# Performance work log

Hardware: AMD Instinct MI355X
Metric: run time of the kernel (lower is better)

The kernel has to match this reference:

```python
import jax, jax.numpy as jnp
import numpy as np

C = 1024
H = 16
DH = C // H
DFF = 4 * C
D = 1024  # cond_dim
B = 2
L = 2048
MAX_SCALE_MUL = float(np.log(100.0))
EPS = 1e-6


def _ln(x):
    # LayerNorm without affine, eps=1e-6
    m = jnp.mean(x, axis=-1, keepdims=True)
    xc = x - m
    var = jnp.mean(xc * xc, axis=-1, keepdims=True)
    return xc * jax.lax.rsqrt(var + EPS)


def setup_inputs() -> dict:
    key = jax.random.key(0)
    ks = jax.random.split(key, 16)
    s = 0.02
    return {
        "x": jax.random.normal(ks[0], (B, L, C), jnp.float32),
        "cond_BD": jax.random.normal(ks[1], (B, D), jnp.float32),
        "attn_bias": jax.random.normal(ks[2], (1, 1, L, L), jnp.float32) * 0.1,
        "qkv_w": jax.random.normal(ks[3], (3 * C, C), jnp.float32) * s,
        "q_bias": jnp.zeros((C,), jnp.float32),
        "v_bias": jnp.zeros((C,), jnp.float32),
        "scale_mul": jnp.full((1, H, 1, 1), np.log(4.0), jnp.float32),
        "proj_w": jax.random.normal(ks[4], (C, C), jnp.float32) * s,
        "proj_b": jnp.zeros((C,), jnp.float32),
        "fc1_w": jax.random.normal(ks[5], (DFF, C), jnp.float32) * s,
        "fc1_b": jnp.zeros((DFF,), jnp.float32),
        "fc2_w": jax.random.normal(ks[6], (C, DFF), jnp.float32) * s,
        "fc2_b": jnp.zeros((C,), jnp.float32),
        "ada_w": jax.random.normal(ks[7], (6 * C, D), jnp.float32) * s,
        "ada_b": jnp.zeros((6 * C,), jnp.float32),
    }


def _attention(x, attn_bias, qkv_w, q_bias, v_bias, scale_mul, proj_w, proj_b):
    b, l, c = x.shape
    bias = jnp.concatenate([q_bias, jnp.zeros_like(q_bias), v_bias])
    qkv = x @ qkv_w.T + bias  # [B,L,3C]
    qkv = qkv.reshape(b, l, 3, H, DH).transpose(2, 0, 3, 1, 4)  # [3,B,H,L,DH]
    q, k, v = qkv[0], qkv[1], qkv[2]
    sm = jnp.exp(jnp.minimum(scale_mul, MAX_SCALE_MUL))  # [1,H,1,1]
    q = q * jax.lax.rsqrt(jnp.sum(q * q, -1, keepdims=True).clip(1e-24)) * sm
    k = k * jax.lax.rsqrt(jnp.sum(k * k, -1, keepdims=True).clip(1e-24))
    attn = jnp.einsum("bhqd,bhkd->bhqk", q, k) + attn_bias
    attn = jax.nn.softmax(attn, axis=-1)
    out = jnp.einsum("bhqk,bhkd->bhqd", attn, v)
    out = out.transpose(0, 2, 1, 3).reshape(b, l, c)
    return out @ proj_w.T + proj_b


def reference(x, cond_BD, attn_bias, qkv_w, q_bias, v_bias, scale_mul,
              proj_w, proj_b, fc1_w, fc1_b, fc2_w, fc2_b, ada_w, ada_b):
    # adaLN modulation: SiLU -> Linear -> 6 chunks of C
    ada = jax.nn.silu(cond_BD) @ ada_w.T + ada_b  # [B,6C]
    ada = ada.reshape(-1, 1, 6, C)
    g1, g2, s1, s2, sh1, sh2 = [ada[:, :, i, :] for i in range(6)]  # each [B,1,C]
    # attention branch
    h = _ln(x) * (s1 + 1.0) + sh1
    x = x + _attention(h, attn_bias, qkv_w, q_bias, v_bias, scale_mul, proj_w, proj_b) * g1
    # FFN branch (GELU tanh approx)
    h = _ln(x) * (s2 + 1.0) + sh2
    h = jax.nn.gelu(h @ fc1_w.T + fc1_b, approximate=True) @ fc2_w.T + fc2_b
    x = x + h * g2
    return x
```

## Files before the change

### kernel.cpp

```cpp
#include <hip/hip_runtime.h>
#include <stdint.h>

#define Ll 2048
#define Mrows 4096
#define LOG2E 1.44269504088896f

typedef unsigned short u16;
typedef __attribute__((ext_vector_type(8))) short short8;
typedef __attribute__((ext_vector_type(4))) float f32x4;

#if __has_builtin(__builtin_amdgcn_exp2f)
#define EXP2F(x) __builtin_amdgcn_exp2f(x)
#else
#define EXP2F(x) exp2f(x)
#endif

__device__ __forceinline__ float b2f(u16 b) {
  union { float f; unsigned u; } x; x.u = ((unsigned)b) << 16; return x.f;
}
__device__ __forceinline__ u16 f2b(float v) {
  union { float f; unsigned u; } x; x.f = v;
  unsigned r = x.u + 0x7fffu + ((x.u >> 16) & 1u);
  return (u16)(r >> 16);
}

#define GLOAD_LDS16(gp, sp)                                                        \
  __builtin_amdgcn_global_load_lds(                                                \
      (__attribute__((address_space(1))) void*)(void*)(gp),                        \
      (__attribute__((address_space(3))) void*)(sp), 16, 0, 0)

__global__ __launch_bounds__(256) void k_convert_all(
    const float* __restrict__ s0, u16* __restrict__ d0,
    const float* __restrict__ s1, u16* __restrict__ d1,
    const float* __restrict__ s2, u16* __restrict__ d2,
    const float* __restrict__ s3, u16* __restrict__ d3,
    const float* __restrict__ s4, float* __restrict__ d4) {
  int i = blockIdx.x * 256 + threadIdx.x;
  if (i >= 3145728) {
    i -= 3145728;
    float4 v = ((const float4*)s4)[i];
    v.x *= LOG2E; v.y *= LOG2E; v.z *= LOG2E; v.w *= LOG2E;
    ((float4*)d4)[i] = v;
    return;
  }
  const float* s; u16* d; int off;
  if (i < 786432)       { s = s0; d = d0; off = 0; }
  else if (i < 1048576) { s = s1; d = d1; off = 786432; }
  else if (i < 2097152) { s = s2; d = d2; off = 1048576; }
  else                  { s = s3; d = d3; off = 2097152; }
  i -= off;
  const float4 v = ((const float4*)s)[i];
  ushort4 o;
  o.x = f2b(v.x); o.y = f2b(v.y); o.z = f2b(v.z); o.w = f2b(v.w);
  ((ushort4*)d)[i] = o;
}

__global__ __launch_bounds__(256) void k_ada(const float* __restrict__ cond,
                                             const float* __restrict__ aw,
                                             const float* __restrict__ ab,
                                             float* __restrict__ out) {
  const int wv = threadIdx.x >> 6, lane = threadIdx.x & 63;
  const int j = blockIdx.x * 4 + wv;
  const int b = j / 6144, jj = j % 6144;
  const float* wr = aw + (size_t)jj * 1024;
  const float* cr = cond + b * 1024;
  float acc = 0.f;
  for (int d = lane; d < 1024; d += 64) {
    const float cv = cr[d];
    acc += (cv / (1.f + __expf(-cv))) * wr[d];
  }
  for (int off = 32; off; off >>= 1) acc += __shfl_xor(acc, off);
  if (lane == 0) out[b * 6144 + jj] = acc + ab[jj];
}

__global__ __launch_bounds__(256) void k_ln_mod(const float* __restrict__ x,
                                                const float* __restrict__ ada,
                                                u16* __restrict__ out,
                                                int s_off, int sh_off) {
  const int row = blockIdx.x;
  const int b = row >> 11;
  const int t = threadIdx.x;
  const float4 xv = ((const float4*)(x + (size_t)row * 1024))[t];
  float s = xv.x + xv.y + xv.z + xv.w;
  float s2 = xv.x * xv.x + xv.y * xv.y + xv.z * xv.z + xv.w * xv.w;
  for (int off = 32; off; off >>= 1) { s += __shfl_xor(s, off); s2 += __shfl_xor(s2, off); }
  __shared__ float red[8];
  const int wv = t >> 6, lane = t & 63;
  if (lane == 0) { red[wv] = s; red[4 + wv] = s2; }
  __syncthreads();
  s = red[0] + red[1] + red[2] + red[3];
  s2 = red[4] + red[5] + red[6] + red[7];
  const float mean = s * (1.f / 1024.f);
  const float var = s2 * (1.f / 1024.f) - mean * mean;
  const float rstd = rsqrtf(var + 1e-6f);
  const float4 sv = ((const float4*)(ada + b * 6144 + s_off))[t];
  const float4 shv = ((const float4*)(ada + b * 6144 + sh_off))[t];
  ushort4 ov;
  ov.x = f2b((xv.x - mean) * rstd * (1.f + sv.x) + shv.x);
  ov.y = f2b((xv.y - mean) * rstd * (1.f + sv.y) + shv.y);
  ov.z = f2b((xv.z - mean) * rstd * (1.f + sv.z) + shv.z);
  ov.w = f2b((xv.w - mean) * rstd * (1.f + sv.w) + shv.w);
  ((ushort4*)(out + (size_t)row * 1024))[t] = ov;
}

__global__ __launch_bounds__(256) void k_resid_ln(const float* __restrict__ x,
                                                  const float* __restrict__ p0,
                                                  const float* __restrict__ p1,
                                                  const float* __restrict__ ada,
                                                  float* __restrict__ x2,
                                                  u16* __restrict__ out) {
  const int row = blockIdx.x;
  const int b = row >> 11;
  const int t = threadIdx.x;
  const float4 xv = ((const float4*)(x + (size_t)row * 1024))[t];
  const float4 pa = ((const float4*)(p0 + (size_t)row * 1024))[t];
  const float4 pb = ((const float4*)(p1 + (size_t)row * 1024))[t];
  const float4 gv = ((const float4*)(ada + b * 6144 + 0))[t];
  float4 v;
  v.x = xv.x + (pa.x + pb.x) * gv.x; v.y = xv.y + (pa.y + pb.y) * gv.y;
  v.z = xv.z + (pa.z + pb.z) * gv.z; v.w = xv.w + (pa.w + pb.w) * gv.w;
  ((float4*)(x2 + (size_t)row * 1024))[t] = v;
  float s = v.x + v.y + v.z + v.w;
  float s2 = v.x * v.x + v.y * v.y + v.z * v.z + v.w * v.w;
  for (int off = 32; off; off >>= 1) { s += __shfl_xor(s, off); s2 += __shfl_xor(s2, off); }
  __shared__ float red[8];
  const int wv = t >> 6, lane = t & 63;
  if (lane == 0) { red[wv] = s; red[4 + wv] = s2; }
  __syncthreads();
  s = red[0] + red[1] + red[2] + red[3];
  s2 = red[4] + red[5] + red[6] + red[7];
  const float mean = s * (1.f / 1024.f);
  const float var = s2 * (1.f / 1024.f) - mean * mean;
  const float rstd = rsqrtf(var + 1e-6f);
  const float4 sv = ((const float4*)(ada + b * 6144 + 3072))[t];
  const float4 shv = ((const float4*)(ada + b * 6144 + 5120))[t];
  ushort4 ov;
  ov.x = f2b((v.x - mean) * rstd * (1.f + sv.x) + shv.x);
  ov.y = f2b((v.y - mean) * rstd * (1.f + sv.y) + shv.y);
  ov.z = f2b((v.z - mean) * rstd * (1.f + sv.z) + shv.z);
  ov.w = f2b((v.w - mean) * rstd * (1.f + sv.w) + shv.w);
  ((ushort4*)(out + (size_t)row * 1024))[t] = ov;
}

__global__ __launch_bounds__(256) void k_final(const float* __restrict__ x2,
                                               const float* __restrict__ f0,
                                               const float* __restrict__ f1,
                                               const float* __restrict__ ada,
                                               float* __restrict__ out) {
  const int i = blockIdx.x * 256 + threadIdx.x;
  const int elem = i * 4;
  const int b = elem >> 21;
  const int c = elem & 1023;
  const float4 xv = ((const float4*)x2)[i];
  const float4 fa = ((const float4*)f0)[i];
  const float4 fb = ((const float4*)f1)[i];
  const float4 gv = *(const float4*)(ada + b * 6144 + 1024 + c);
  float4 ov;
  ov.x = xv.x + (fa.x + fb.x) * gv.x; ov.y = xv.y + (fa.y + fb.y) * gv.y;
  ov.z = xv.z + (fa.z + fb.z) * gv.z; ov.w = xv.w + (fa.w + fb.w) * gv.w;
  ((float4*)out)[i] = ov;
}

template <int OUT_BF16, int GELU_ACT>
__global__ __launch_bounds__(256, 2)
void k_gemm_bt(const u16* __restrict__ A, const u16* __restrict__ W,
               const float* __restrict__ bias, void* __restrict__ Cout,
               float* __restrict__ Cout2, int M, int N, int Kc) {
  __shared__ u16 As[128 * 64];
  __shared__ u16 Bs[128 * 64];
  const int tid = threadIdx.x;
  const int wv = tid >> 6;
  const int lane = tid & 63;
  const int q = lane >> 4;
  const int r = lane & 15;
  const int wm = (wv & 1) * 64;
  const int wn = (wv >> 1) * 64;
  const int m0 = blockIdx.x * 128;
  const int n0 = blockIdx.y * 128;
  const int K = Kc * gridDim.z;
  const int kt0 = blockIdx.z * Kc;

  f32x4 acc[4][4];
#pragma unroll
  for (int i = 0; i < 4; ++i)
#pragma unroll
    for (int j = 0; j < 4; ++j) acc[i][j] = (f32x4)0.0f;

  const int srow = tid >> 3;
  const int scol = (tid & 7) * 8;
  const u16* Ag = A + (size_t)(m0 + srow) * K + scol;
  const u16* Wg = W + (size_t)(n0 + srow) * K + scol;
  u16* AsBase = &As[wv * 512];
  u16* BsBase = &Bs[wv * 512];

  for (int kt = kt0; kt < kt0 + Kc; kt += 64) {
    __syncthreads();
#pragma unroll
    for (int p = 0; p < 4; ++p) {
      GLOAD_LDS16(Ag + (size_t)(p * 32) * K + kt, AsBase + p * 2048);
      GLOAD_LDS16(Wg + (size_t)(p * 32) * K + kt, BsBase + p * 2048);
    }
    __syncthreads();
#pragma unroll
    for (int kc = 0; kc < 2; ++kc) {
      short8 af[4], bfr[4];
#pragma unroll
      for (int i = 0; i < 4; ++i) {
        af[i] = *(const short8*)(As + (wm + i * 16 + r) * 64 + kc * 32 + q * 8);
        bfr[i] = *(const short8*)(Bs + (wn + i * 16 + r) * 64 + kc * 32 + q * 8);
      }
#pragma unroll
      for (int mi = 0; mi < 4; ++mi)
#pragma unroll
        for (int ni = 0; ni < 4; ++ni)
          acc[mi][ni] = __builtin_amdgcn_mfma_f32_16x16x32_bf16(af[mi], bfr[ni],
                                                                acc[mi][ni], 0, 0, 0);
    }
  }
  float* Cf = (blockIdx.z == 0) ? (float*)Cout : Cout2;
#pragma unroll
  for (int mi = 0; mi < 4; ++mi) {
#pragma unroll
    for (int ni = 0; ni < 4; ++ni) {
      const int col = n0 + wn + ni * 16 + r;
      const float bv = (blockIdx.z == 0) ? bias[col] : 0.f;
#pragma unroll
      for (int rr = 0; rr < 4; ++rr) {
        const int rowg = m0 + wm + mi * 16 + q * 4 + rr;
        float v = acc[mi][ni][rr] + bv;
        if (GELU_ACT) {
          const float t = tanhf(0.7978845608028654f * (v + 0.044715f * v * v * v));
          v = 0.5f * v * (1.0f + t);
        }
        if (OUT_BF16)
          ((u16*)Cout)[(size_t)rowg * N + col] = f2b(v);
        else
          Cf[(size_t)rowg * N + col] = v;
      }
    }
  }
}

__global__ __launch_bounds__(256, 2)
void k_gemm_qkv(const u16* __restrict__ A, const u16* __restrict__ W,
                const float* __restrict__ qb, const float* __restrict__ vb,
                const float* __restrict__ scale_mul, u16* __restrict__ Cout) {
  const int N = 3072, K = 1024;
  __shared__ u16 As[128 * 64];
  __shared__ u16 Bs[128 * 64];
  const int tid = threadIdx.x;
  const int wv = tid >> 6;
  const int lane = tid & 63;
  const int q = lane >> 4;
  const int r = lane & 15;
  const int wm = (wv & 1) * 64;
  const int wn = (wv >> 1) * 64;
  const int m0 = blockIdx.x * 128;
  const int n0 = blockIdx.y * 128;

  f32x4 acc[4][4];
#pragma unroll
  for (int i = 0; i < 4; ++i)
#pragma unroll
    for (int j = 0; j < 4; ++j) acc[i][j] = (f32x4)0.0f;

  const int srow = tid >> 3;
  const int scol = (tid & 7) * 8;
  const u16* Ag = A + (size_t)(m0 + srow) * K + scol;
  const u16* Wg = W + (size_t)(n0 + srow) * K + scol;
  u16* AsBase = &As[wv * 512];
  u16* BsBase = &Bs[wv * 512];

  for (int kt = 0; kt < K; kt += 64) {
    __syncthreads();
#pragma unroll
    for (int p = 0; p < 4; ++p) {
      GLOAD_LDS16(Ag + (size_t)(p * 32) * K + kt, AsBase + p * 2048);
      GLOAD_LDS16(Wg + (size_t)(p * 32) * K + kt, BsBase + p * 2048);
    }
    __syncthreads();
#pragma unroll
    for (int kc = 0; kc < 2; ++kc) {
      short8 af[4], bfr[4];
#pragma unroll
      for (int i = 0; i < 4; ++i) {
        af[i] = *(const short8*)(As + (wm + i * 16 + r) * 64 + kc * 32 + q * 8);
        bfr[i] = *(const short8*)(Bs + (wn + i * 16 + r) * 64 + kc * 32 + q * 8);
      }
#pragma unroll
      for (int mi = 0; mi < 4; ++mi)
#pragma unroll
        for (int ni = 0; ni < 4; ++ni)
          acc[mi][ni] = __builtin_amdgcn_mfma_f32_16x16x32_bf16(af[mi], bfr[ni],
                                                                acc[mi][ni], 0, 0, 0);
    }
  }
  const int cb = n0 + wn;
  const int sec = cb >> 10;
  const int hh = (cb >> 6) & 15;
  const float sm = (sec == 0)
      ? __expf(fminf(scale_mul[hh], 4.605170185988091f)) * LOG2E : 1.f;
#pragma unroll
  for (int mi = 0; mi < 4; ++mi) {
    float v[4][4];
#pragma unroll
    for (int ni = 0; ni < 4; ++ni) {
      const int d = ni * 16 + r;
      const float bvv = (sec == 0) ? qb[(cb & 1023) + d]
                        : (sec == 2 ? vb[(cb & 1023) + d] : 0.f);
#pragma unroll
      for (int rr = 0; rr < 4; ++rr) v[ni][rr] = acc[mi][ni][rr] + bvv;
    }
    if (sec < 2) {
#pragma unroll
      for (int rr = 0; rr < 4; ++rr) {
        float ss = v[0][rr] * v[0][rr] + v[1][rr] * v[1][rr] +
                   v[2][rr] * v[2][rr] + v[3][rr] * v[3][rr];
        ss += __shfl_xor(ss, 1); ss += __shfl_xor(ss, 2);
        ss += __shfl_xor(ss, 4); ss += __shfl_xor(ss, 8);
        const float sc = rsqrtf(fmaxf(ss, 1e-24f)) * sm;
#pragma unroll
        for (int ni = 0; ni < 4; ++ni) v[ni][rr] *= sc;
      }
    }
#pragma unroll
    for (int ni = 0; ni < 4; ++ni) {
      const int col = cb + ni * 16 + r;
#pragma unroll
      for (int rr = 0; rr < 4; ++rr) {
        const int rowg = m0 + wm + mi * 16 + q * 4 + rr;
        Cout[(size_t)rowg * N + col] = f2b(v[ni][rr]);
      }
    }
  }
}

__global__ __launch_bounds__(512)
void k_flash(const u16* __restrict__ qkv, const float* __restrict__ bl2e,
             u16* __restrict__ o) {
  __shared__ u16 Qs[128 * 64];
  __shared__ u16 Ks[2][64 * 64];
  __shared__ u16 Vt[2][64 * 72];
  __shared__ u16 Ps[8][16 * 72];
  __shared__ float stat[8][16];
  const int tid = threadIdx.x;
  const int bh = blockIdx.x;
  const int qb = blockIdx.y;
  const int b = bh >> 4, h = bh & 15;
  const int wv = tid >> 6, lane = tid & 63;
  const int quad = lane >> 4, c = lane & 15;
  const u16* Qg = qkv + (size_t)b * Ll * 3072 + h * 64;
  const u16* Kg = Qg + 1024;
  const u16* Vg = Qg + 2048;
  const int srow = tid >> 3, scol = (tid & 7) * 8;
  const int vc = tid & 15, va = (tid >> 4) & 1, vd0 = (tid >> 5) * 4;

  {
    const u16* gp = Qg + (size_t)(qb * 128 + srow) * 3072 + scol;
    GLOAD_LDS16(gp, &Qs[wv * 512]);
    GLOAD_LDS16(gp + (size_t)64 * 3072, &Qs[4096 + wv * 512]);
  }

  f32x4 O[4];
  float lacc[4];
#pragma unroll
  for (int i = 0; i < 4; ++i) { O[i] = (f32x4)0.f; lacc[i] = 0.f; }
  const float* bb = bl2e + (size_t)(qb * 128 + wv * 16 + quad * 4) * 2048 + c;

  float bA[4][4], bB[4][4];
  GLOAD_LDS16(Kg + (size_t)srow * 3072 + scol, &Ks[0][wv * 512]);
  {
    const u16* vp = Vg + (size_t)(va * 32 + vc) * 3072 + vd0;
    const ushort4 r0 = *(const ushort4*)vp;
    const ushort4 r1 = *(const ushort4*)(vp + (size_t)16 * 3072);
    u16* vt = &Vt[0][vd0 * 72 + vc * 4 + va * 2];
    *(unsigned*)(vt + 0 * 72) = (unsigned)r0.x | ((unsigned)r1.x << 16);
    *(unsigned*)(vt + 1 * 72) = (unsigned)r0.y | ((unsigned)r1.y << 16);
    *(unsigned*)(vt + 2 * 72) = (unsigned)r0.z | ((unsigned)r1.z << 16);
    *(unsigned*)(vt + 3 * 72) = (unsigned)r0.w | ((unsigned)r1.w << 16);
  }
#pragma unroll
  for (int ni = 0; ni < 4; ++ni)
#pragma unroll
    for (int rr = 0; rr < 4; ++rr) bA[ni][rr] = bb[rr * 2048 + ni * 16];

  auto tile = [&](int kt, u16* KsC, u16* KsN, u16* VtC, u16* VtN,
                  float (&bC)[4][4], float (&bN)[4][4]) __attribute__((always_inline)) {
    const int ktn = (kt < 31) ? kt + 1 : 31;
    __syncthreads();
    GLOAD_LDS16(Kg + (size_t)(ktn * 64 + srow) * 3072 + scol, &KsN[wv * 512]);
    ushort4 vr0, vr1;
    {
      const u16* vp = Vg + (size_t)(ktn * 64 + va * 32 + vc) * 3072 + vd0;
      vr0 = *(const ushort4*)vp;
      vr1 = *(const ushort4*)(vp + (size_t)16 * 3072);
    }
#pragma unroll
    for (int ni = 0; ni < 4; ++ni)
#pragma unroll
      for (int rr = 0; rr < 4; ++rr)
        bN[ni][rr] = bb[rr * 2048 + ktn * 64 + ni * 16];
    f32x4 S[4];
#pragma unroll
    for (int ni = 0; ni < 4; ++ni)
#pragma unroll
      for (int rr = 0; rr < 4; ++rr) S[ni][rr] = bC[ni][rr];
#pragma unroll
    for (int ks = 0; ks < 2; ++ks) {
      const short8 aq = *(const short8*)(&Qs[(wv * 16 + c) * 64 + ks * 32 + quad * 8]);
#pragma unroll
      for (int ni = 0; ni < 4; ++ni) {
        const short8 bk = *(const short8*)(&KsC[(ni * 16 + c) * 64 + ks * 32 + quad * 8]);
        S[ni] = __builtin_amdgcn_mfma_f32_16x16x32_bf16(aq, bk, S[ni], 0, 0, 0);
      }
    }
#pragma unroll
    for (int rr = 0; rr < 4; ++rr) {
      union { float f; unsigned u; } p0, p1, p2, p3;
      p0.f = EXP2F(S[0][rr]); p1.f = EXP2F(S[1][rr]);
      p2.f = EXP2F(S[2][rr]); p3.f = EXP2F(S[3][rr]);
      lacc[rr] += (p0.f + p1.f) + (p2.f + p3.f);
      uint2 pk;
      pk.x = __builtin_amdgcn_perm(p1.u + 0x8000u, p0.u + 0x8000u, 0x07060302u);
      pk.y = __builtin_amdgcn_perm(p3.u + 0x8000u, p2.u + 0x8000u, 0x07060302u);
      *(uint2*)(&Ps[wv][(quad * 4 + rr) * 72 + c * 4]) = pk;
    }
    __threadfence_block();
#pragma unroll
    for (int ks = 0; ks < 2; ++ks) {
      const short8 bp = *(const short8*)(&Ps[wv][c * 72 + ks * 32 + quad * 8]);
#pragma unroll
      for (int i = 0; i < 4; ++i) {
        const short8 av = *(const short8*)(&VtC[(i * 16 + c) * 72 + ks * 32 + quad * 8]);
        O[i] = __builtin_amdgcn_mfma_f32_16x16x32_bf16(av, bp, O[i], 0, 0, 0);
      }
    }
    {
      u16* vt = &VtN[vd0 * 72 + vc * 4 + va * 2];
      *(unsigned*)(vt + 0 * 72) = (unsigned)vr0.x | ((unsigned)vr1.x << 16);
      *(unsigned*)(vt + 1 * 72) = (unsigned)vr0.y | ((unsigned)vr1.y << 16);
      *(unsigned*)(vt + 2 * 72) = (unsigned)vr0.z | ((unsigned)vr1.z << 16);
      *(unsigned*)(vt + 3 * 72) = (unsigned)vr0.w | ((unsigned)vr1.w << 16);
    }
  };

  for (int kt = 0; kt < 32; kt += 2) {
    tile(kt,     Ks[0], Ks[1], Vt[0], Vt[1], bA, bB);
    tile(kt + 1, Ks[1], Ks[0], Vt[1], Vt[0], bB, bA);
  }

#pragma unroll
  for (int rr = 0; rr < 4; ++rr) {
    float l = lacc[rr];
    l += __shfl_xor(l, 1); l += __shfl_xor(l, 2);
    l += __shfl_xor(l, 4); l += __shfl_xor(l, 8);
    lacc[rr] = l;
  }
  if (c == 0)
    *(float4*)(&stat[wv][quad * 4]) = make_float4(lacc[0], lacc[1], lacc[2], lacc[3]);
  __threadfence_block();
  const float inv = 1.f / stat[wv][c];
  u16* op = o + (size_t)(b * Ll + qb * 128 + wv * 16 + c) * 1024 + h * 64;
#pragma unroll
  for (int i = 0; i < 4; ++i) {
    ushort4 ov;
    ov.x = f2b(O[i][0] * inv); ov.y = f2b(O[i][1] * inv);
    ov.z = f2b(O[i][2] * inv); ov.w = f2b(O[i][3] * inv);
    *(ushort4*)(op + i * 16 + quad * 4) = ov;
  }
}

extern "C" void kernel_launch(void* const* d_in, const int* in_sizes, int n_in,
                              void* d_out, int out_size, void* d_ws, size_t ws_size,
                              hipStream_t stream) {
  const float* x = (const float*)d_in[0];
  const float* cond = (const float*)d_in[1];
  const float* attn_bias = (const float*)d_in[2];
  const float* qkv_w = (const float*)d_in[3];
  const float* q_bias = (const float*)d_in[4];
  const float* v_bias = (const float*)d_in[5];
  const float* scale_mul = (const float*)d_in[6];
  const float* proj_w = (const float*)d_in[7];
  const float* proj_b = (const float*)d_in[8];
  const float* fc1_w = (const float*)d_in[9];
  const float* fc1_b = (const float*)d_in[10];
  const float* fc2_w = (const float*)d_in[11];
  const float* fc2_b = (const float*)d_in[12];
  const float* ada_w = (const float*)d_in[13];
  const float* ada_b = (const float*)d_in[14];
  float* out = (float*)d_out;
  char* ws = (char*)d_ws;

  float* ada_out = (float*)(ws + 0);
  u16* wqkv = (u16*)(ws + 61440);
  u16* wproj = (u16*)(ws + 6352896);
  u16* wfc1 = (u16*)(ws + 8450048);
  u16* wfc2 = (u16*)(ws + 16838656);
  u16* sb = (u16*)(ws + 25227264);
  u16* big = (u16*)(ws + 33615872);
  float* g32 = (float*)(ws + 67170304);
  float* x2 = (float*)(ws + 83947520);
  float* bl2e = x2;
  float* projp0 = (float*)big;
  float* projp1 = (float*)(big + (size_t)8 * 1024 * 1024);
  float* fc2p1 = (float*)(ws + 61440);

  k_convert_all<<<16384, 256, 0, stream>>>(qkv_w, wqkv, proj_w, wproj,
                                           fc1_w, wfc1, fc2_w, wfc2,
                                           attn_bias, bl2e);
  k_ada<<<3072, 256, 0, stream>>>(cond, ada_w, ada_b, ada_out);
  k_ln_mod<<<4096, 256, 0, stream>>>(x, ada_out, sb, 2048, 4096);
  k_gemm_qkv<<<dim3(32, 24), 256, 0, stream>>>(sb, wqkv, q_bias, v_bias,
                                               scale_mul, big);
  k_flash<<<dim3(32, 16), 512, 0, stream>>>(big, bl2e, sb);
  k_gemm_bt<0, 0><<<dim3(32, 8, 2), 256, 0, stream>>>(sb, wproj, proj_b, projp0,
                                                      projp1, Mrows, 1024, 512);
  k_resid_ln<<<4096, 256, 0, stream>>>(x, projp0, projp1, ada_out, x2, sb);
  k_gemm_bt<1, 1><<<dim3(32, 32, 1), 256, 0, stream>>>(sb, wfc1, fc1_b, big,
                                                       nullptr, Mrows, 4096, 1024);
  k_gemm_bt<0, 0><<<dim3(32, 8, 2), 256, 0, stream>>>(big, wfc2, fc2_b, g32,
                                                      fc2p1, Mrows, 1024, 2048);
  k_final<<<4096, 256, 0, stream>>>(x2, g32, fc2p1, ada_out, out);
}
```

Baseline: 432.9 us.

## Double-buffer GEMM LDS tiles, XOR-swizzle LDS layout, store attention bias as bf16

Both GEMM kernels now double-buffer their LDS tiles, so the next K-tile's global-to-LDS load is issued before the current tile is computed, and one barrier per iteration is removed. The GEMMs and the flash kernel use an XOR swizzle on LDS columns to reduce bank conflicts on the MFMA fragment reads. The pre-scaled attention bias is stored as bf16 instead of fp32, which halves the bias traffic read by the flash kernel but lowers the bias to bf16 precision. Doubling the LDS footprint may reduce GEMM occupancy.

```diff
diff --git a/kernel.cpp b/kernel.cpp
--- a/kernel.cpp
+++ b/kernel.cpp
@@ -34,13 +34,15 @@
     const float* __restrict__ s1, u16* __restrict__ d1,
     const float* __restrict__ s2, u16* __restrict__ d2,
     const float* __restrict__ s3, u16* __restrict__ d3,
-    const float* __restrict__ s4, float* __restrict__ d4) {
+    const float* __restrict__ s4, u16* __restrict__ d4) {
   int i = blockIdx.x * 256 + threadIdx.x;
   if (i >= 3145728) {
     i -= 3145728;
-    float4 v = ((const float4*)s4)[i];
-    v.x *= LOG2E; v.y *= LOG2E; v.z *= LOG2E; v.w *= LOG2E;
-    ((float4*)d4)[i] = v;
+    const float4 v = ((const float4*)s4)[i];
+    ushort4 o;
+    o.x = f2b(v.x * LOG2E); o.y = f2b(v.y * LOG2E);
+    o.z = f2b(v.z * LOG2E); o.w = f2b(v.w * LOG2E);
+    ((ushort4*)d4)[i] = o;
     return;
   }
   const float* s; u16* d; int off;
@@ -166,8 +168,8 @@
 void k_gemm_bt(const u16* __restrict__ A, const u16* __restrict__ W,
                const float* __restrict__ bias, void* __restrict__ Cout,
                float* __restrict__ Cout2, int M, int N, int Kc) {
-  __shared__ u16 As[128 * 64];
-  __shared__ u16 Bs[128 * 64];
+  __shared__ u16 As[2][128 * 64];
+  __shared__ u16 Bs[2][128 * 64];
   const int tid = threadIdx.x;
   const int wv = tid >> 6;
   const int lane = tid & 63;
@@ -187,27 +189,34 @@
     for (int j = 0; j < 4; ++j) acc[i][j] = (f32x4)0.0f;
 
   const int srow = tid >> 3;
-  const int scol = (tid & 7) * 8;
+  const int scol = ((tid & 7) ^ (srow & 7)) * 8;
   const u16* Ag = A + (size_t)(m0 + srow) * K + scol;
   const u16* Wg = W + (size_t)(n0 + srow) * K + scol;
-  u16* AsBase = &As[wv * 512];
-  u16* BsBase = &Bs[wv * 512];
-
-  for (int kt = kt0; kt < kt0 + Kc; kt += 64) {
+  const int sw = r & 7;
+
+  auto stage = [&](int kt, int buf) __attribute__((always_inline)) {
+#pragma unroll
+    for (int p = 0; p < 4; ++p) {
+      GLOAD_LDS16(Ag + (size_t)(p * 32) * K + kt, &As[buf][wv * 512 + p * 2048]);
+      GLOAD_LDS16(Wg + (size_t)(p * 32) * K + kt, &Bs[buf][wv * 512 + p * 2048]);
+    }
+  };
+
+  const int nt = Kc >> 6;
+  stage(kt0, 0);
+  for (int it = 0; it < nt; ++it) {
+    const int cur = it & 1;
     __syncthreads();
-#pragma unroll
-    for (int p = 0; p < 4; ++p) {
-      GLOAD_LDS16(Ag + (size_t)(p * 32) * K + kt, AsBase + p * 2048);
-      GLOAD_LDS16(Wg + (size_t)(p * 32) * K + kt, BsBase + p * 2048);
-    }
-    __syncthreads();
+    if (it + 1 < nt) stage(kt0 + (it + 1) * 64, cur ^ 1);
+    const u16* AsC = As[cur];
+    const u16* BsC = Bs[cur];
 #pragma unroll
     for (int kc = 0; kc < 2; ++kc) {
       short8 af[4], bfr[4];
 #pragma unroll
       for (int i = 0; i < 4; ++i) {
-        af[i] = *(const short8*)(As + (wm + i * 16 + r) * 64 + kc * 32 + q * 8);
-        bfr[i] = *(const short8*)(Bs + (wn + i * 16 + r) * 64 + kc * 32 + q * 8);
+        af[i] = *(const short8*)(&AsC[(wm + i * 16 + r) * 64 + ((kc * 4 + q) ^ sw) * 8]);
+        bfr[i] = *(const short8*)(&BsC[(wn + i * 16 + r) * 64 + ((kc * 4 + q) ^ sw) * 8]);
       }
 #pragma unroll
       for (int mi = 0; mi < 4; ++mi)
@@ -246,8 +255,8 @@
                 const float* __restrict__ qb, const float* __restrict__ vb,
                 const float* __restrict__ scale_mul, u16* __restrict__ Cout) {
   const int N = 3072, K = 1024;
-  __shared__ u16 As[128 * 64];
-  __shared__ u16 Bs[128 * 64];
+  __shared__ u16 As[2][128 * 64];
+  __shared__ u16 Bs[2][128 * 64];
   const int tid = threadIdx.x;
   const int wv = tid >> 6;
   const int lane = tid & 63;
@@ -265,27 +274,33 @@
     for (int j = 0; j < 4; ++j) acc[i][j] = (f32x4)0.0f;
 
   const int srow = tid >> 3;
-  const int scol = (tid & 7) * 8;
+  const int scol = ((tid & 7) ^ (srow & 7)) * 8;
   const u16* Ag = A + (size_t)(m0 + srow) * K + scol;
   const u16* Wg = W + (size_t)(n0 + srow) * K + scol;
-  u16* AsBase = &As[wv * 512];
-  u16* BsBase = &Bs[wv * 512];
-
-  for (int kt = 0; kt < K; kt += 64) {
+  const int sw = r & 7;
+
+  auto stage = [&](int kt, int buf) __attribute__((always_inline)) {
+#pragma unroll
+    for (int p = 0; p < 4; ++p) {
+      GLOAD_LDS16(Ag + (size_t)(p * 32) * K + kt, &As[buf][wv * 512 + p * 2048]);
+      GLOAD_LDS16(Wg + (size_t)(p * 32) * K + kt, &Bs[buf][wv * 512 + p * 2048]);
+    }
+  };
+
+  stage(0, 0);
+  for (int it = 0; it < 16; ++it) {
+    const int cur = it & 1;
     __syncthreads();
-#pragma unroll
-    for (int p = 0; p < 4; ++p) {
-      GLOAD_LDS16(Ag + (size_t)(p * 32) * K + kt, AsBase + p * 2048);
-      GLOAD_LDS16(Wg + (size_t)(p * 32) * K + kt, BsBase + p * 2048);
-    }
-    __syncthreads();
+    if (it + 1 < 16) stage((it + 1) * 64, cur ^ 1);
+    const u16* AsC = As[cur];
+    const u16* BsC = Bs[cur];
 #pragma unroll
     for (int kc = 0; kc < 2; ++kc) {
       short8 af[4], bfr[4];
 #pragma unroll
       for (int i = 0; i < 4; ++i) {
-        af[i] = *(const short8*)(As + (wm + i * 16 + r) * 64 + kc * 32 + q * 8);
-        bfr[i] = *(const short8*)(Bs + (wn + i * 16 + r) * 64 + kc * 32 + q * 8);
+        af[i] = *(const short8*)(&AsC[(wm + i * 16 + r) * 64 + ((kc * 4 + q) ^ sw) * 8]);
+        bfr[i] = *(const short8*)(&BsC[(wn + i * 16 + r) * 64 + ((kc * 4 + q) ^ sw) * 8]);
       }
 #pragma unroll
       for (int mi = 0; mi < 4; ++mi)
@@ -336,7 +351,7 @@
 }
 
 __global__ __launch_bounds__(512)
-void k_flash(const u16* __restrict__ qkv, const float* __restrict__ bl2e,
+void k_flash(const u16* __restrict__ qkv, const u16* __restrict__ bias16,
              u16* __restrict__ o) {
   __shared__ u16 Qs[128 * 64];
   __shared__ u16 Ks[2][64 * 64];
@@ -352,8 +367,10 @@
   const u16* Qg = qkv + (size_t)b * Ll * 3072 + h * 64;
   const u16* Kg = Qg + 1024;
   const u16* Vg = Qg + 2048;
-  const int srow = tid >> 3, scol = (tid & 7) * 8;
+  const int srow = tid >> 3;
+  const int scol = ((tid & 7) ^ (srow & 7)) * 8;
   const int vc = tid & 15, va = (tid >> 4) & 1, vd0 = (tid >> 5) * 4;
+  const int swc = c & 7;
 
   {
     const u16* gp = Qg + (size_t)(qb * 128 + srow) * 3072 + scol;
@@ -365,9 +382,9 @@
   float lacc[4];
 #pragma unroll
   for (int i = 0; i < 4; ++i) { O[i] = (f32x4)0.f; lacc[i] = 0.f; }
-  const float* bb = bl2e + (size_t)(qb * 128 + wv * 16 + quad * 4) * 2048 + c;
-
-  float bA[4][4], bB[4][4];
+  const u16* bb = bias16 + (size_t)(qb * 128 + wv * 16 + quad * 4) * 2048 + c;
+
+  u16 bA[4][4], bB[4][4];
   GLOAD_LDS16(Kg + (size_t)srow * 3072 + scol, &Ks[0][wv * 512]);
   {
     const u16* vp = Vg + (size_t)(va * 32 + vc) * 3072 + vd0;
@@ -385,7 +402,7 @@
     for (int rr = 0; rr < 4; ++rr) bA[ni][rr] = bb[rr * 2048 + ni * 16];
 
   auto tile = [&](int kt, u16* KsC, u16* KsN, u16* VtC, u16* VtN,
-                  float (&bC)[4][4], float (&bN)[4][4]) __attribute__((always_inline)) {
+                  u16 (&bC)[4][4], u16 (&bN)[4][4]) __attribute__((always_inline)) {
     const int ktn = (kt < 31) ? kt + 1 : 31;
     __syncthreads();
     GLOAD_LDS16(Kg + (size_t)(ktn * 64 + srow) * 3072 + scol, &KsN[wv * 512]);
@@ -404,13 +421,15 @@
 #pragma unroll
     for (int ni = 0; ni < 4; ++ni)
 #pragma unroll
-      for (int rr = 0; rr < 4; ++rr) S[ni][rr] = bC[ni][rr];
+      for (int rr = 0; rr < 4; ++rr) S[ni][rr] = b2f(bC[ni][rr]);
 #pragma unroll
     for (int ks = 0; ks < 2; ++ks) {
-      const short8 aq = *(const short8*)(&Qs[(wv * 16 + c) * 64 + ks * 32 + quad * 8]);
+      const short8 aq =
+          *(const short8*)(&Qs[(wv * 16 + c) * 64 + ((ks * 4 + quad) ^ swc) * 8]);
 #pragma unroll
       for (int ni = 0; ni < 4; ++ni) {
-        const short8 bk = *(const short8*)(&KsC[(ni * 16 + c) * 64 + ks * 32 + quad * 8]);
+        const short8 bk =
+            *(const short8*)(&KsC[(ni * 16 + c) * 64 + ((ks * 4 + quad) ^ swc) * 8]);
         S[ni] = __builtin_amdgcn_mfma_f32_16x16x32_bf16(aq, bk, S[ni], 0, 0, 0);
       }
     }
@@ -500,19 +519,19 @@
   u16* big = (u16*)(ws + 33615872);
   float* g32 = (float*)(ws + 67170304);
   float* x2 = (float*)(ws + 83947520);
-  float* bl2e = x2;
+  u16* wbias = big + (size_t)4096 * 3072;
   float* projp0 = (float*)big;
   float* projp1 = (float*)(big + (size_t)8 * 1024 * 1024);
   float* fc2p1 = (float*)(ws + 61440);
 
   k_convert_all<<<16384, 256, 0, stream>>>(qkv_w, wqkv, proj_w, wproj,
                                            fc1_w, wfc1, fc2_w, wfc2,
-                                           attn_bias, bl2e);
+                                           attn_bias, wbias);
   k_ada<<<3072, 256, 0, stream>>>(cond, ada_w, ada_b, ada_out);
   k_ln_mod<<<4096, 256, 0, stream>>>(x, ada_out, sb, 2048, 4096);
   k_gemm_qkv<<<dim3(32, 24), 256, 0, stream>>>(sb, wqkv, q_bias, v_bias,
                                                scale_mul, big);
-  k_flash<<<dim3(32, 16), 512, 0, stream>>>(big, bl2e, sb);
+  k_flash<<<dim3(32, 16), 512, 0, stream>>>(big, wbias, sb);
   k_gemm_bt<0, 0><<<dim3(32, 8, 2), 256, 0, stream>>>(sb, wproj, proj_b, projp0,
                                                       projp1, Mrows, 1024, 512);
   k_resid_ln<<<4096, 256, 0, stream>>>(x, projp0, projp1, ada_out, x2, sb);
```

Result: slower. 444.0 us (+2.6%).
